# Kernel optimization log

Hardware: AMD Instinct MI355X
Metric: run time of the kernel (lower is better)

The kernel has to match this reference:

```python
import jax, jax.numpy as jnp
import numpy as np

N, C_S, C_Z, H, D = 512, 384, 128, 16, 24  # c_hidden per head
EPS = 1e-5

def _ln(x, g, b):
    m = jnp.mean(x, axis=-1, keepdims=True)
    v = jnp.mean(jnp.square(x - m), axis=-1, keepdims=True)
    return (x - m) * jax.lax.rsqrt(v + EPS) * g + b

def setup_inputs() -> dict:
    key = jax.random.key(0)
    ks = jax.random.split(key, 12)
    s = lambda fan: 1.0 / np.sqrt(fan)
    return {
        "a": jax.random.normal(ks[0], (1, N, C_S), jnp.float32),
        "z": jax.random.normal(ks[1], (1, N, N, C_Z), jnp.float32),
        "g_a": jnp.ones((C_S,), jnp.float32),
        "b_a": jnp.zeros((C_S,), jnp.float32),
        "g_z": jnp.ones((C_Z,), jnp.float32),
        "b_z": jnp.zeros((C_Z,), jnp.float32),
        "Wz": jax.random.normal(ks[2], (C_Z, H), jnp.float32) * s(C_Z),
        "bz": jnp.zeros((H,), jnp.float32),
        "Wq": jax.random.normal(ks[3], (C_S, H * D), jnp.float32) * s(C_S),
        "Wk": jax.random.normal(ks[4], (C_S, H * D), jnp.float32) * s(C_S),
        "Wv": jax.random.normal(ks[5], (C_S, H * D), jnp.float32) * s(C_S),
        "Wg": jax.random.normal(ks[6], (C_S, H * D), jnp.float32) * s(C_S),
        "bg": jnp.zeros((H * D,), jnp.float32),
        "Wo": jax.random.normal(ks[7], (H * D, C_S), jnp.float32) * s(H * D),
        "bo": jnp.zeros((C_S,), jnp.float32),
    }

def reference(a, z, g_a, b_a, g_z, b_z, Wz, bz, Wq, Wk, Wv, Wg, bg, Wo, bo):
    B = a.shape[0]
    a_n = _ln(a, g_a, b_a)                       # [B,N,C_S]
    z_n = _ln(z, g_z, b_z)                       # [B,N,N,C_Z]
    # linear_z then permute(0,3,1,2): [B,N,N,H] -> [B,H,N,N]
    pair_bias = jnp.einsum('bijc,ch->bhij', z_n, Wz) + bz[None, :, None, None]
    q = (a_n @ Wq).reshape(B, N, H, D) * (1.0 / np.sqrt(D))
    k = (a_n @ Wk).reshape(B, N, H, D)
    v = (a_n @ Wv).reshape(B, N, H, D)
    scores = jnp.einsum('bqhd,bkhd->bhqk', q, k) + pair_bias
    p = jax.nn.softmax(scores, axis=-1)
    o = jnp.einsum('bhqk,bkhd->bqhd', p, v)      # [B,N,H,D]
    g = jax.nn.sigmoid(a_n @ Wg + bg).reshape(B, N, H, D)
    o = (o * g).reshape(B, N, H * D)
    return o @ Wo + bo                            # [B,N,C_S]
```

## Files before the change

### kernel.cpp

```cpp
#include <hip/hip_runtime.h>
#include <math.h>

#define N 512
#define CS 384
#define CZ 128
#define NH 16
#define DH 24
#define HD 384
#define NN (N*N)
#define EPS 1e-5f

#define OFF_AN   0
#define OFF_QT   196608
#define OFF_KT   393216
#define OFF_VT   589824
#define OFF_GT   786432
#define OFF_OG   983040
#define OFF_WZ2  1179648
#define OFF_SH   1181696
#define OFF_BH   1181712
#define OFF_BIAS 1181728

__global__ void __launch_bounds__(256) ln_prep_kernel(const float* __restrict__ a, const float* __restrict__ g_a,
                                                      const float* __restrict__ b_a, float* __restrict__ an_out,
                                                      const float* __restrict__ g_z, const float* __restrict__ lnb_z,
                                                      const float* __restrict__ Wz, const float* __restrict__ bz,
                                                      float* __restrict__ wz2, float* __restrict__ sh,
                                                      float* __restrict__ bh) {
    __shared__ float ls[NH][17], lb[NH][17];
    __shared__ float l1[4], l2[4];
    const int t = threadIdx.x;
    if (blockIdx.x == 256) {
        for (int i = t; i < NH * CZ; i += 256) {
            int h = i >> 7, c = i & (CZ - 1);
            wz2[h * CZ + c] = g_z[c] * Wz[c * NH + h];
        }
        int h = t >> 4, seg = t & 15;
        float s = 0.f, b = 0.f;
        #pragma unroll
        for (int i = 0; i < 8; ++i) {
            int c = seg * 8 + i;
            float w = Wz[c * NH + h];
            s += g_z[c] * w;
            b += lnb_z[c] * w;
        }
        ls[h][seg] = s; lb[h][seg] = b;
        __syncthreads();
        if (t < NH) {
            float ss = 0.f, bb = 0.f;
            #pragma unroll
            for (int i = 0; i < 16; ++i) { ss += ls[t][i]; bb += lb[t][i]; }
            sh[t] = ss;
            bh[t] = bb + bz[t];
        }
        return;
    }
    const int half = t >> 7;
    const int tr = t & 127;
    const int r = blockIdx.x * 2 + half;
    const float* row = a + r * CS;
    float x0 = row[tr], x1 = row[tr + 128], x2 = row[tr + 256];
    float s1 = x0 + x1 + x2;
    float s2 = x0 * x0 + x1 * x1 + x2 * x2;
    #pragma unroll
    for (int m = 1; m < 64; m <<= 1) {
        s1 += __shfl_xor(s1, m, 64);
        s2 += __shfl_xor(s2, m, 64);
    }
    if ((t & 63) == 0) { l1[t >> 6] = s1; l2[t >> 6] = s2; }
    __syncthreads();
    s1 = l1[half * 2] + l1[half * 2 + 1];
    s2 = l2[half * 2] + l2[half * 2 + 1];
    float mu = s1 * (1.f / CS);
    float var = s2 * (1.f / CS) - mu * mu;
    float rs = rsqrtf(var + EPS);
    float* an = an_out + r * CS;
    an[tr]       = (x0 - mu) * rs * g_a[tr]       + b_a[tr];
    an[tr + 128] = (x1 - mu) * rs * g_a[tr + 128] + b_a[tr + 128];
    an[tr + 256] = (x2 - mu) * rs * g_a[tr + 256] + b_a[tr + 256];
}

__global__ void __launch_bounds__(256) qkvg_kernel(const float* __restrict__ Wq, const float* __restrict__ Wk,
                                                   const float* __restrict__ Wv, const float* __restrict__ Wg,
                                                   const float* __restrict__ bg, const float* __restrict__ an,
                                                   float* __restrict__ qt, float* __restrict__ kt,
                                                   float* __restrict__ vt, float* __restrict__ gt) {
    const int lane = threadIdx.x & 63;
    const int w = __builtin_amdgcn_readfirstlane(threadIdx.x >> 6);
    const int strip = blockIdx.x * 4 + w;
    const int n0 = strip * 8;
    const int sel = n0 / HD;
    const int col = n0 % HD;
    const float* Wm = (sel == 0) ? Wq : (sel == 1) ? Wk : (sel == 2) ? Wv : Wg;
    const int m = blockIdx.y * 64 + lane;
    const float* arow = an + m * CS;
    float acc[8];
    #pragma unroll
    for (int j = 0; j < 8; ++j) acc[j] = 0.f;
    for (int kb = 0; kb < CS; kb += 32) {
        float4 av[8];
        #pragma unroll
        for (int i = 0; i < 8; ++i) av[i] = ((const float4*)(arow + kb))[i];
        #pragma unroll
        for (int i = 0; i < 8; ++i) {
            const float* wr = Wm + (kb + i * 4) * HD + col;
            #pragma unroll
            for (int j = 0; j < 8; ++j) {
                acc[j] += av[i].x * wr[j];
                acc[j] += av[i].y * wr[HD + j];
                acc[j] += av[i].z * wr[2 * HD + j];
                acc[j] += av[i].w * wr[3 * HD + j];
            }
        }
    }
    float* dst = (sel == 0) ? qt : (sel == 1) ? kt : (sel == 2) ? vt : gt;
    if (sel == 3) {
        #pragma unroll
        for (int j = 0; j < 8; ++j) acc[j] = 1.f / (1.f + __expf(-(acc[j] + bg[col + j])));
    } else if (sel == 0) {
        #pragma unroll
        for (int j = 0; j < 8; ++j) acc[j] *= 0.20412414523193153f;
    }
    #pragma unroll
    for (int j = 0; j < 8; ++j) {
        int c = col + j;
        int h = c / DH, d = c % DH;
        dst[(h * N + m) * DH + d] = acc[j];
    }
}

__global__ void __launch_bounds__(256) pairbias_kernel(const float* __restrict__ z,
                                                       const float* __restrict__ wz2,
                                                       const float* __restrict__ sh,
                                                       const float* __restrict__ bh,
                                                       float* __restrict__ bias) {
    const int lane = threadIdx.x & 63;
    const int w = threadIdx.x >> 6;
    const int r4 = lane >> 4;
    const int cl = lane & 15;
    const int wave_row0 = blockIdx.x * 128 + w * 32;
    const float shc = sh[cl];
    const float bhc = bh[cl];
    for (int g = 0; g < 8; ++g) {
        const int row = wave_row0 + g * 4 + r4;
        const float* zr = z + (size_t)row * CZ + cl * 8;
        float4 z0 = ((const float4*)zr)[0];
        float4 z1 = ((const float4*)zr)[1];
        float s1 = z0.x + z0.y + z0.z + z0.w + z1.x + z1.y + z1.z + z1.w;
        float s2 = z0.x*z0.x + z0.y*z0.y + z0.z*z0.z + z0.w*z0.w
                 + z1.x*z1.x + z1.y*z1.y + z1.z*z1.z + z1.w*z1.w;
        float dots[NH];
        #pragma unroll
        for (int h = 0; h < NH; ++h) {
            const float4* wp = (const float4*)(wz2 + h * CZ + cl * 8);
            float4 w0 = wp[0], w1 = wp[1];
            dots[h] = z0.x*w0.x + z0.y*w0.y + z0.z*w0.z + z0.w*w0.w
                    + z1.x*w1.x + z1.y*w1.y + z1.z*w1.z + z1.w*w1.w;
        }
        #pragma unroll
        for (int m = 1; m < 16; m <<= 1) {
            s1 += __shfl_xor(s1, m, 64);
            s2 += __shfl_xor(s2, m, 64);
            #pragma unroll
            for (int h = 0; h < NH; ++h) dots[h] += __shfl_xor(dots[h], m, 64);
        }
        float mu = s1 * (1.f / CZ);
        float var = s2 * (1.f / CZ) - mu * mu;
        float rr = rsqrtf(var + EPS);
        float d = dots[0];
        #pragma unroll
        for (int h = 1; h < NH; ++h) d = (cl == h) ? dots[h] : d;
        bias[cl * NN + row] = rr * (d - mu * shc) + bhc;
    }
}

__global__ void __launch_bounds__(256) attn_kernel(const float* __restrict__ qt, const float* __restrict__ kt,
                                                   const float* __restrict__ vt, const float* __restrict__ gt,
                                                   const float* __restrict__ bias, float* __restrict__ og) {
    const int lane = threadIdx.x & 63;
    const int w = __builtin_amdgcn_readfirstlane(threadIdx.x >> 6);
    const int qhalf = lane >> 5;
    const int klane = lane & 31;
    const int h = blockIdx.y;
    const int q = blockIdx.x * 8 + w * 2 + qhalf;
    const float* qT = qt + h * N * DH;
    const float* kT = kt + h * N * DH;
    const float* vT = vt + h * N * DH;

    float qv[DH];
    #pragma unroll
    for (int d6 = 0; d6 < 6; ++d6) {
        float4 t4 = ((const float4*)(qT + q * DH))[d6];
        qv[d6 * 4 + 0] = t4.x; qv[d6 * 4 + 1] = t4.y; qv[d6 * 4 + 2] = t4.z; qv[d6 * 4 + 3] = t4.w;
    }
    float sc[16];
    #pragma unroll
    for (int t = 0; t < 16; ++t) {
        const int kk = t * 32 + klane;
        const float4* kr = (const float4*)(kT + kk * DH);
        float4 k0 = kr[0], k1 = kr[1], k2 = kr[2], k3 = kr[3], k4 = kr[4], k5 = kr[5];
        float s = qv[0]*k0.x + qv[1]*k0.y + qv[2]*k0.z + qv[3]*k0.w
                + qv[4]*k1.x + qv[5]*k1.y + qv[6]*k1.z + qv[7]*k1.w
                + qv[8]*k2.x + qv[9]*k2.y + qv[10]*k2.z + qv[11]*k2.w
                + qv[12]*k3.x + qv[13]*k3.y + qv[14]*k3.z + qv[15]*k3.w
                + qv[16]*k4.x + qv[17]*k4.y + qv[18]*k4.z + qv[19]*k4.w
                + qv[20]*k5.x + qv[21]*k5.y + qv[22]*k5.z + qv[23]*k5.w;
        sc[t] = s + bias[h * NN + q * N + kk];
    }
    float mx = sc[0];
    #pragma unroll
    for (int t = 1; t < 16; ++t) mx = fmaxf(mx, sc[t]);
    #pragma unroll
    for (int m = 1; m < 32; m <<= 1) mx = fmaxf(mx, __shfl_xor(mx, m, 64));
    float sum = 0.f;
    #pragma unroll
    for (int t = 0; t < 16; ++t) { sc[t] = __expf(sc[t] - mx); sum += sc[t]; }
    #pragma unroll
    for (int m = 1; m < 32; m <<= 1) sum += __shfl_xor(sum, m, 64);
    float inv = 1.f / sum;
    #pragma unroll
    for (int t = 0; t < 16; ++t) sc[t] *= inv;
    float acc[DH];
    #pragma unroll
    for (int d = 0; d < DH; ++d) acc[d] = 0.f;
    #pragma unroll
    for (int t = 0; t < 16; ++t) {
        const int kk = t * 32 + klane;
        const float4* vr = (const float4*)(vT + kk * DH);
        float4 v0 = vr[0], v1 = vr[1], v2 = vr[2], v3 = vr[3], v4 = vr[4], v5 = vr[5];
        float p = sc[t];
        acc[0] += p*v0.x;  acc[1] += p*v0.y;  acc[2] += p*v0.z;  acc[3] += p*v0.w;
        acc[4] += p*v1.x;  acc[5] += p*v1.y;  acc[6] += p*v1.z;  acc[7] += p*v1.w;
        acc[8] += p*v2.x;  acc[9] += p*v2.y;  acc[10] += p*v2.z; acc[11] += p*v2.w;
        acc[12] += p*v3.x; acc[13] += p*v3.y; acc[14] += p*v3.z; acc[15] += p*v3.w;
        acc[16] += p*v4.x; acc[17] += p*v4.y; acc[18] += p*v4.z; acc[19] += p*v4.w;
        acc[20] += p*v5.x; acc[21] += p*v5.y; acc[22] += p*v5.z; acc[23] += p*v5.w;
    }
    #pragma unroll
    for (int m = 1; m < 32; m <<= 1) {
        #pragma unroll
        for (int d = 0; d < DH; ++d) acc[d] += __shfl_xor(acc[d], m, 64);
    }
    float o = 0.f;
    #pragma unroll
    for (int d = 0; d < DH; ++d) o = (klane == d) ? acc[d] : o;
    if (klane < DH) {
        float g = gt[h * N * DH + q * DH + klane];
        og[q * HD + h * DH + klane] = o * g;
    }
}

__global__ void __launch_bounds__(256) out_gemm_kernel(const float* __restrict__ Wo, const float* __restrict__ bo,
                                                       const float* __restrict__ og, float* __restrict__ out) {
    const int lane = threadIdx.x & 63;
    const int w = __builtin_amdgcn_readfirstlane(threadIdx.x >> 6);
    const int strip = blockIdx.x * 4 + w;
    const int c0 = strip * 4;
    const int m = blockIdx.y * 64 + lane;
    const float* orow = og + m * HD;
    float acc[4];
    #pragma unroll
    for (int j = 0; j < 4; ++j) acc[j] = 0.f;
    for (int kb = 0; kb < HD; kb += 32) {
        float4 av[8];
        #pragma unroll
        for (int i = 0; i < 8; ++i) av[i] = ((const float4*)(orow + kb))[i];
        #pragma unroll
        for (int i = 0; i < 8; ++i) {
            const float* wr = Wo + (kb + i * 4) * CS + c0;
            #pragma unroll
            for (int j = 0; j < 4; ++j) {
                acc[j] += av[i].x * wr[j];
                acc[j] += av[i].y * wr[CS + j];
                acc[j] += av[i].z * wr[2 * CS + j];
                acc[j] += av[i].w * wr[3 * CS + j];
            }
        }
    }
    #pragma unroll
    for (int j = 0; j < 4; ++j) out[m * CS + c0 + j] = acc[j] + bo[c0 + j];
}

extern "C" void kernel_launch(void* const* d_in, const int* in_sizes, int n_in,
                              void* d_out, int out_size, void* d_ws, size_t ws_size,
                              hipStream_t stream) {
    const float* a    = (const float*)d_in[0];
    const float* z    = (const float*)d_in[1];
    const float* g_a  = (const float*)d_in[2];
    const float* b_a  = (const float*)d_in[3];
    const float* g_z  = (const float*)d_in[4];
    const float* b_z  = (const float*)d_in[5];
    const float* Wz   = (const float*)d_in[6];
    const float* bz   = (const float*)d_in[7];
    const float* Wq   = (const float*)d_in[8];
    const float* Wk   = (const float*)d_in[9];
    const float* Wv   = (const float*)d_in[10];
    const float* Wg   = (const float*)d_in[11];
    const float* bg   = (const float*)d_in[12];
    const float* Wo   = (const float*)d_in[13];
    const float* bo   = (const float*)d_in[14];
    float* ws  = (float*)d_ws;
    float* out = (float*)d_out;

    float* an   = ws + OFF_AN;
    float* qt   = ws + OFF_QT;
    float* kt   = ws + OFF_KT;
    float* vt   = ws + OFF_VT;
    float* gt   = ws + OFF_GT;
    float* ogp  = ws + OFF_OG;
    float* wz2  = ws + OFF_WZ2;
    float* shp  = ws + OFF_SH;
    float* bhp  = ws + OFF_BH;
    float* bias = ws + OFF_BIAS;

    hipLaunchKernelGGL(ln_prep_kernel, dim3(257),    dim3(256), 0, stream,
                       a, g_a, b_a, an, g_z, b_z, Wz, bz, wz2, shp, bhp);
    hipLaunchKernelGGL(qkvg_kernel,    dim3(48, 8),  dim3(256), 0, stream,
                       Wq, Wk, Wv, Wg, bg, an, qt, kt, vt, gt);
    hipLaunchKernelGGL(pairbias_kernel, dim3(2048),  dim3(256), 0, stream,
                       z, wz2, shp, bhp, bias);
    hipLaunchKernelGGL(attn_kernel,    dim3(64, 16), dim3(256), 0, stream,
                       qt, kt, vt, gt, bias, ogp);
    hipLaunchKernelGGL(out_gemm_kernel, dim3(24, 8), dim3(256), 0, stream,
                       Wo, bo, ogp, out);
}
```

Before: 356.4 us.

## Stage z tiles in LDS and compute pair bias per row without shuffles

The pair-bias kernel now loads a 128-row tile of z into shared memory with an XOR swizzle. Each thread then owns one row and eight heads, accumulating LayerNorm statistics and head dot products serially. This removes the 16-head cross-lane shuffle reductions and the redundant per-lane dot products. It also makes the bias stores coalesced across rows. In exchange it uses 64KB of LDS per block, which limits occupancy, and each thread does a longer serial loop with wave-uniform weight loads.

```diff
diff --git a/kernel.cpp b/kernel.cpp
--- a/kernel.cpp
+++ b/kernel.cpp
@@ -134,44 +134,45 @@
                                                        const float* __restrict__ sh,
                                                        const float* __restrict__ bh,
                                                        float* __restrict__ bias) {
-    const int lane = threadIdx.x & 63;
-    const int w = threadIdx.x >> 6;
-    const int r4 = lane >> 4;
-    const int cl = lane & 15;
-    const int wave_row0 = blockIdx.x * 128 + w * 32;
-    const float shc = sh[cl];
-    const float bhc = bh[cl];
-    for (int g = 0; g < 8; ++g) {
-        const int row = wave_row0 + g * 4 + r4;
-        const float* zr = z + (size_t)row * CZ + cl * 8;
-        float4 z0 = ((const float4*)zr)[0];
-        float4 z1 = ((const float4*)zr)[1];
-        float s1 = z0.x + z0.y + z0.z + z0.w + z1.x + z1.y + z1.z + z1.w;
-        float s2 = z0.x*z0.x + z0.y*z0.y + z0.z*z0.z + z0.w*z0.w
-                 + z1.x*z1.x + z1.y*z1.y + z1.z*z1.z + z1.w*z1.w;
-        float dots[NH];
-        #pragma unroll
-        for (int h = 0; h < NH; ++h) {
-            const float4* wp = (const float4*)(wz2 + h * CZ + cl * 8);
-            float4 w0 = wp[0], w1 = wp[1];
-            dots[h] = z0.x*w0.x + z0.y*w0.y + z0.z*w0.z + z0.w*w0.w
-                    + z1.x*w1.x + z1.y*w1.y + z1.z*w1.z + z1.w*w1.w;
-        }
-        #pragma unroll
-        for (int m = 1; m < 16; m <<= 1) {
-            s1 += __shfl_xor(s1, m, 64);
-            s2 += __shfl_xor(s2, m, 64);
-            #pragma unroll
-            for (int h = 0; h < NH; ++h) dots[h] += __shfl_xor(dots[h], m, 64);
-        }
-        float mu = s1 * (1.f / CZ);
-        float var = s2 * (1.f / CZ) - mu * mu;
-        float rr = rsqrtf(var + EPS);
-        float d = dots[0];
-        #pragma unroll
-        for (int h = 1; h < NH; ++h) d = (cl == h) ? dots[h] : d;
-        bias[cl * NN + row] = rr * (d - mu * shc) + bhc;
-    }
+    __shared__ float4 lz[128 * 32];
+    const int t = threadIdx.x;
+    const int r_l = t & 127;
+    const int hg = __builtin_amdgcn_readfirstlane(t >> 7);
+    const int h0 = hg * 8;
+    const int row0 = blockIdx.x * 128;
+
+    const float4* zsrc = (const float4*)(z + (size_t)row0 * CZ);
+    #pragma unroll
+    for (int i = 0; i < 16; ++i) {
+        const int g4 = i * 256 + t;
+        float4 v = zsrc[g4];
+        const int r = g4 >> 5, cc = g4 & 31;
+        lz[r * 32 + (cc ^ (r & 31))] = v;
+    }
+    __syncthreads();
+
+    float s1 = 0.f, s2 = 0.f;
+    float dots[8];
+    #pragma unroll
+    for (int j = 0; j < 8; ++j) dots[j] = 0.f;
+    #pragma unroll 8
+    for (int cc = 0; cc < 32; ++cc) {
+        float4 v = lz[r_l * 32 + (cc ^ (r_l & 31))];
+        s1 += v.x + v.y + v.z + v.w;
+        s2 += v.x * v.x + v.y * v.y + v.z * v.z + v.w * v.w;
+        #pragma unroll
+        for (int j = 0; j < 8; ++j) {
+            const float4 wv = ((const float4*)(wz2 + (h0 + j) * CZ))[cc];
+            dots[j] += v.x * wv.x + v.y * wv.y + v.z * wv.z + v.w * wv.w;
+        }
+    }
+    const float mu = s1 * (1.f / CZ);
+    const float var = s2 * (1.f / CZ) - mu * mu;
+    const float rr = rsqrtf(var + EPS);
+    const int row = row0 + r_l;
+    #pragma unroll
+    for (int j = 0; j < 8; ++j)
+        bias[(h0 + j) * NN + row] = rr * (dots[j] - mu * sh[h0 + j]) + bh[h0 + j];
 }
 
 __global__ void __launch_bounds__(256) attn_kernel(const float* __restrict__ qt, const float* __restrict__ kt,
```

Result: no change. 349.5 us (-1.9%).
